# Kernel optimization log

Hardware: AMD Instinct MI355X
Metric: run time of the kernel (lower is better)

Reference implementation:

```python
import jax, jax.numpy as jnp
import numpy as np
import math

B, S, D, H, DFF = 4, 1024, 1024, 16, 4096
DK = D // H
EPS = 1e-6


def setup_inputs() -> dict:
    key = jax.random.key(0)
    ks = jax.random.split(key, 8)
    sc = 1.0 / math.sqrt(D)
    return {
        "x": jax.random.normal(ks[0], (B, S, D), jnp.float32),
        "src_mask": jnp.ones((B, 1, 1, S), jnp.int32),
        "wq": jax.random.normal(ks[1], (D, D), jnp.float32) * sc,
        "bq": jnp.zeros((D,), jnp.float32),
        "wk": jax.random.normal(ks[2], (D, D), jnp.float32) * sc,
        "bk": jnp.zeros((D,), jnp.float32),
        "wv": jax.random.normal(ks[3], (D, D), jnp.float32) * sc,
        "bv": jnp.zeros((D,), jnp.float32),
        "wo": jax.random.normal(ks[4], (D, D), jnp.float32) * sc,
        "bo": jnp.zeros((D,), jnp.float32),
        "w1": jax.random.normal(ks[5], (D, DFF), jnp.float32) * sc,
        "b1": jnp.zeros((DFF,), jnp.float32),
        "w2": jax.random.normal(ks[6], (DFF, D), jnp.float32) * (1.0 / math.sqrt(DFF)),
        "b2": jnp.zeros((D,), jnp.float32),
        "alpha1": jnp.ones((1,), jnp.float32),
        "beta1": jnp.zeros((1,), jnp.float32),
        "alpha2": jnp.ones((1,), jnp.float32),
        "beta2": jnp.zeros((1,), jnp.float32),
    }


def layer_norm(x, alpha, beta):
    # Faithful to the custom LayerNormalization: scalar alpha/beta,
    # torch std (unbiased, ddof=1), eps added to std (not variance).
    mean = jnp.mean(x, axis=-1, keepdims=True)
    std = jnp.std(x, axis=-1, keepdims=True, ddof=1)
    return alpha * (x - mean) / (std + EPS) + beta


def encoder_block(x, src_mask, wq, bq, wk, bk, wv, bv, wo, bo,
                  w1, b1, w2, b2, alpha1, beta1, alpha2, beta2):
    # --- residual 1: pre-norm self-attention (dropout = 0 / eval mode) ---
    xn = layer_norm(x, alpha1, beta1)
    q = (xn @ wq + bq).reshape(B, S, H, DK).transpose(0, 2, 1, 3)  # bhsd
    k = (xn @ wk + bk).reshape(B, S, H, DK).transpose(0, 2, 1, 3)
    v = (xn @ wv + bv).reshape(B, S, H, DK).transpose(0, 2, 1, 3)
    scores = jnp.einsum("bhqd,bhkd->bhqk", q, k) / math.sqrt(DK)
    scores = jnp.where(src_mask == 0, jnp.float32(-1e9), scores)
    attn = jax.nn.softmax(scores, axis=-1)
    ctx = jnp.einsum("bhqk,bhkd->bhqd", attn, v)
    ctx = ctx.transpose(0, 2, 1, 3).reshape(B, S, D)
    x = x + (ctx @ wo + bo)
    # --- residual 2: pre-norm feed-forward ---
    xn2 = layer_norm(x, alpha2, beta2)
    ff = jax.nn.relu(xn2 @ w1 + b1) @ w2 + b2
    return x + ff


def reference(x, src_mask, wq, bq, wk, bk, wv, bv, wo, bo,
              w1, b1, w2, b2, alpha1, beta1, alpha2, beta2):
    return encoder_block(x, src_mask, wq, bq, wk, bk, wv, bv, wo, bo,
                         w1, b1, w2, b2, alpha1, beta1, alpha2, beta2)
```

## Files before the change

### kernel.cpp

```cpp
#include <hip/hip_runtime.h>
#include <hip/hip_bf16.h>
#include <stdint.h>


typedef unsigned short u16;
typedef __attribute__((ext_vector_type(4))) float f32x4;
typedef __attribute__((ext_vector_type(8))) short bf16x8;
typedef __attribute__((ext_vector_type(4))) unsigned short u16x4;

__device__ __forceinline__ u16 f2b(float f) {
  unsigned int u = __builtin_bit_cast(unsigned int, f);
  u += 0x7FFFu + ((u >> 16) & 1u);
  return (u16)(u >> 16);
}

__device__ __forceinline__ void gload_lds16(const void* g, void* l) {
  __builtin_amdgcn_global_load_lds(
      reinterpret_cast<__attribute__((address_space(1))) void*>(
          reinterpret_cast<uintptr_t>(g)),
      reinterpret_cast<__attribute__((address_space(3))) void*>(
          reinterpret_cast<uintptr_t>(l)),
      16, 0, 0);
}

#define MFMA16(a, b, c) __builtin_amdgcn_mfma_f32_16x16x32_bf16((a), (b), (c), 0, 0, 0)

__global__ __launch_bounds__(256) void cast_transpose(
    const float* __restrict__ in, u16* __restrict__ out, int K, int N) {
  __shared__ float tile[32][33];
  const int n0 = blockIdx.x * 32, k0 = blockIdx.y * 32;
  const int tx = threadIdx.x & 31, ty = threadIdx.x >> 5;
#pragma unroll
  for (int i = 0; i < 32; i += 8)
    tile[ty + i][tx] = in[(int64_t)(k0 + ty + i) * N + (n0 + tx)];
  __syncthreads();
#pragma unroll
  for (int i = 0; i < 32; i += 8)
    out[(int64_t)(n0 + ty + i) * K + (k0 + tx)] = f2b(tile[tx][ty + i]);
}

__global__ void pack_bias(const float* __restrict__ bq, const float* __restrict__ bk,
                          const float* __restrict__ bv, float* __restrict__ out) {
  int i = blockIdx.x * 256 + threadIdx.x;
  const float* src = (i < 1024) ? bq : (i < 2048 ? bk : bv);
  out[i] = src[i & 1023];
}

__global__ __launch_bounds__(256) void transpose_v(
    const u16* __restrict__ qkv, u16* __restrict__ vt) {
  __shared__ u16 t[32][33];
  const int bh = blockIdx.z;
  const int b = bh >> 4, h = bh & 15;
  const int s0 = blockIdx.x * 32, d0 = blockIdx.y * 32;
  const int tx = threadIdx.x & 31, ty = threadIdx.x >> 5;
  const u16* src = qkv + (int64_t)(b * 1024) * 3072 + 2048 + h * 64;
#pragma unroll
  for (int i = 0; i < 32; i += 8)
    t[ty + i][tx] = src[(int64_t)(s0 + ty + i) * 3072 + d0 + tx];
  __syncthreads();
  u16* dst = vt + (int64_t)bh * 64 * 1024;
#pragma unroll
  for (int i = 0; i < 32; i += 8)
    dst[(int64_t)(d0 + ty + i) * 1024 + s0 + tx] = t[tx][ty + i];
}

__global__ __launch_bounds__(256) void layernorm_k(
    const float* __restrict__ x, const float* __restrict__ alpha,
    const float* __restrict__ beta, u16* __restrict__ out) {
  const int row = blockIdx.x;
  const float4 v = ((const float4*)(x + (int64_t)row * 1024))[threadIdx.x];
  float s = v.x + v.y + v.z + v.w;
  float sq = v.x * v.x + v.y * v.y + v.z * v.z + v.w * v.w;
#pragma unroll
  for (int off = 1; off < 64; off <<= 1) {
    s += __shfl_xor(s, off, 64);
    sq += __shfl_xor(sq, off, 64);
  }
  __shared__ float ss[4], ssq[4];
  const int wid = threadIdx.x >> 6;
  if ((threadIdx.x & 63) == 0) { ss[wid] = s; ssq[wid] = sq; }
  __syncthreads();
  s = ss[0] + ss[1] + ss[2] + ss[3];
  sq = ssq[0] + ssq[1] + ssq[2] + ssq[3];
  const float mean = s * (1.0f / 1024.0f);
  float var = (sq - 1024.0f * mean * mean) * (1.0f / 1023.0f);
  var = fmaxf(var, 0.0f);
  const float inv = alpha[0] / (sqrtf(var) + 1e-6f);
  const float bt = beta[0];
  u16x4 o;
  o[0] = f2b((v.x - mean) * inv + bt);
  o[1] = f2b((v.y - mean) * inv + bt);
  o[2] = f2b((v.z - mean) * inv + bt);
  o[3] = f2b((v.w - mean) * inv + bt);
  *(u16x4*)(out + (int64_t)row * 1024 + threadIdx.x * 4) = o;
}

template <int BN, bool OUT_BF16, bool RELU, bool RES>
__global__ __launch_bounds__(256) void gemm_bt(
    const u16* __restrict__ A, const u16* __restrict__ Bt,
    const float* __restrict__ bias, const float* __restrict__ res,
    void* __restrict__ Cout, int Ndim, int K) {
  constexpr int NF = BN / 32;
  __shared__ u16 Alds[128 * 32];
  __shared__ u16 Blds[BN * 32];
  const int tid = threadIdx.x;
  const int wid = tid >> 6, lane = tid & 63;
  const int bm0 = blockIdx.y * 128, bn0 = blockIdx.x * BN;
  const int wm = (wid >> 1) * 64, wn = (wid & 1) * (BN / 2);
  const int lrow = lane & 15, lg = lane >> 4;

  f32x4 acc[4][NF] = {};

  const int srow = tid >> 2;
  const int skoff = (tid & 3) * 8;
  const u16* Ag = A + (int64_t)(bm0 + srow) * K + skoff;
  const u16* Bg = Bt + (int64_t)(bn0 + srow) * K + skoff;
  char* AldsB0 = (char*)Alds + wid * 64 * 16;
  char* AldsB1 = (char*)Alds + (256 + wid * 64) * 16;
  char* BldsB0 = (char*)Blds + wid * 64 * 16;
  char* BldsB1 = (char*)Blds + (256 + wid * 64) * 16;
  const int64_t half = (int64_t)64 * K;

  const int nK = K >> 5;
  for (int kt = 0; kt < nK; ++kt) {
    __syncthreads();
    gload_lds16(Ag, AldsB0);
    gload_lds16(Ag + half, AldsB1);
    gload_lds16(Bg, BldsB0);
    if (BN == 128) gload_lds16(Bg + half, BldsB1);
    Ag += 32; Bg += 32;
    __syncthreads();
    bf16x8 af[4], bfr[NF];
#pragma unroll
    for (int f = 0; f < 4; ++f)
      af[f] = *(const bf16x8*)&Alds[(wm + f * 16 + lrow) * 32 + lg * 8];
#pragma unroll
    for (int f = 0; f < NF; ++f)
      bfr[f] = *(const bf16x8*)&Blds[(wn + f * 16 + lrow) * 32 + lg * 8];
#pragma unroll
    for (int mf = 0; mf < 4; ++mf)
#pragma unroll
      for (int nf = 0; nf < NF; ++nf)
        acc[mf][nf] = MFMA16(af[mf], bfr[nf], acc[mf][nf]);
  }

#pragma unroll
  for (int mf = 0; mf < 4; ++mf) {
#pragma unroll
    for (int nf = 0; nf < NF; ++nf) {
      const int col = bn0 + wn + nf * 16 + lrow;
      const float bv = bias[col];
#pragma unroll
      for (int r = 0; r < 4; ++r) {
        const int row = bm0 + wm + mf * 16 + lg * 4 + r;
        float v = acc[mf][nf][r] + bv;
        if (RELU) v = fmaxf(v, 0.0f);
        if (RES) v += res[(int64_t)row * Ndim + col];
        if (OUT_BF16)
          ((u16*)Cout)[(int64_t)row * Ndim + col] = f2b(v);
        else
          ((float*)Cout)[(int64_t)row * Ndim + col] = v;
      }
    }
  }
}

__global__ __launch_bounds__(256) void attention_k(
    const u16* __restrict__ qkv, const u16* __restrict__ vt,
    const int* __restrict__ mask, u16* __restrict__ ctxout) {
  const int bh = blockIdx.y;
  const int b = bh >> 4, h = bh & 15;
  const int q0 = blockIdx.x * 64;
  const int tid = threadIdx.x, wid = tid >> 6, lane = tid & 63;
  const int lrow = lane & 15, lg = lane >> 4;

  __shared__ u16 Klds[64 * 64];
  __shared__ u16 Vtlds[64 * 64];
  __shared__ u16 Plds[4][16 * 68];

  const int64_t rs = 3072;
  const u16* Qb = qkv + (int64_t)(b * 1024) * rs + h * 64;
  const u16* Kb = Qb + 1024;
  const u16* Vtb = vt + (int64_t)bh * 64 * 1024;

  bf16x8 qf[2];
  {
    const u16* qp = Qb + (int64_t)(q0 + wid * 16 + lrow) * rs + lg * 8;
    qf[0] = *(const bf16x8*)qp;
    qf[1] = *(const bf16x8*)(qp + 32);
  }

  const int c0 = wid * 64 + lane, c1 = 256 + c0;
  const int r0 = c0 >> 3, r1 = c1 >> 3;
  const int gq0 = (c0 & 7) ^ (r0 & 7), gq1 = (c1 & 7) ^ (r1 & 7);
  char* KldsB0 = (char*)Klds + wid * 64 * 16;
  char* KldsB1 = (char*)Klds + (256 + wid * 64) * 16;
  char* VldsB0 = (char*)Vtlds + wid * 64 * 16;
  char* VldsB1 = (char*)Vtlds + (256 + wid * 64) * 16;
  const u16* Kg0 = Kb + (int64_t)r0 * rs + gq0 * 8;
  const u16* Kg1 = Kb + (int64_t)r1 * rs + gq1 * 8;
  const u16* Vg0 = Vtb + r0 * 1024 + gq0 * 8;
  const u16* Vg1 = Vtb + r1 * 1024 + gq1 * 8;

  float m[4], l[4];
  f32x4 ctx[4] = {};
#pragma unroll
  for (int r = 0; r < 4; ++r) { m[r] = -1e30f; l[r] = 0.0f; }

  for (int kt = 0; kt < 16; ++kt) {
    const int sk0 = kt * 64;
    __syncthreads();
    gload_lds16(Kg0 + (int64_t)sk0 * rs, KldsB0);
    gload_lds16(Kg1 + (int64_t)sk0 * rs, KldsB1);
    gload_lds16(Vg0 + sk0, VldsB0);
    gload_lds16(Vg1 + sk0, VldsB1);
    __syncthreads();

    f32x4 sa[4];
#pragma unroll
    for (int nf = 0; nf < 4; ++nf) {
      const int srow = nf * 16 + lrow;
      const char* kr = (const char*)Klds + srow * 128;
      bf16x8 kf0 = *(const bf16x8*)(kr + ((lg ^ (srow & 7)) * 16));
      bf16x8 kf1 = *(const bf16x8*)(kr + (((4 | lg) ^ (srow & 7)) * 16));
      f32x4 a = {};
      a = MFMA16(qf[0], kf0, a);
      a = MFMA16(qf[1], kf1, a);
      sa[nf] = a;
    }
#pragma unroll
    for (int nf = 0; nf < 4; ++nf) {
      const int mval = mask[b * 1024 + sk0 + nf * 16 + lrow];
#pragma unroll
      for (int r = 0; r < 4; ++r) {
        const float sv = sa[nf][r] * 0.125f;
        sa[nf][r] = (mval == 0) ? -1e9f : sv;
      }
    }
    float fac[4];
#pragma unroll
    for (int r = 0; r < 4; ++r) {
      float mx = fmaxf(fmaxf(sa[0][r], sa[1][r]), fmaxf(sa[2][r], sa[3][r]));
#pragma unroll
      for (int off = 1; off < 16; off <<= 1) mx = fmaxf(mx, __shfl_xor(mx, off, 64));
      const float mn = fmaxf(m[r], mx);
      fac[r] = __expf(m[r] - mn);
      m[r] = mn;
    }
    float rsum[4] = {0.f, 0.f, 0.f, 0.f};
    u16 pb[4][4];
#pragma unroll
    for (int nf = 0; nf < 4; ++nf)
#pragma unroll
      for (int r = 0; r < 4; ++r) {
        const float p = __expf(sa[nf][r] - m[r]);
        rsum[r] += p;
        pb[nf][r] = f2b(p);
      }
#pragma unroll
    for (int r = 0; r < 4; ++r) {
      float t = rsum[r];
#pragma unroll
      for (int off = 1; off < 16; off <<= 1) t += __shfl_xor(t, off, 64);
      l[r] = l[r] * fac[r] + t;
#pragma unroll
      for (int df = 0; df < 4; ++df) ctx[df][r] *= fac[r];
    }
    u16* P = &Plds[wid][0];
#pragma unroll
    for (int nf = 0; nf < 4; ++nf)
#pragma unroll
      for (int r = 0; r < 4; ++r)
        P[(lg * 4 + r) * 68 + nf * 16 + lrow] = pb[nf][r];
    bf16x8 pf0 = *(const bf16x8*)&P[lrow * 68 + lg * 8];
    bf16x8 pf1 = *(const bf16x8*)&P[lrow * 68 + 32 + lg * 8];
#pragma unroll
    for (int df = 0; df < 4; ++df) {
      const int drow = df * 16 + lrow;
      const char* vr = (const char*)Vtlds + drow * 128;
      bf16x8 vf0 = *(const bf16x8*)(vr + ((lg ^ (drow & 7)) * 16));
      bf16x8 vf1 = *(const bf16x8*)(vr + (((4 | lg) ^ (drow & 7)) * 16));
      ctx[df] = MFMA16(pf0, vf0, ctx[df]);
      ctx[df] = MFMA16(pf1, vf1, ctx[df]);
    }
  }
#pragma unroll
  for (int df = 0; df < 4; ++df)
#pragma unroll
    for (int r = 0; r < 4; ++r) {
      const int row = b * 1024 + q0 + wid * 16 + lg * 4 + r;
      const int col = h * 64 + df * 16 + lrow;
      ctxout[(int64_t)row * 1024 + col] = f2b(ctx[df][r] / l[r]);
    }
}

extern "C" void kernel_launch(void* const* d_in, const int* in_sizes, int n_in,
                              void* d_out, int out_size, void* d_ws, size_t ws_size,
                              hipStream_t stream) {
  (void)in_sizes; (void)n_in; (void)out_size; (void)ws_size;
  const float* x      = (const float*)d_in[0];
  const int*   mask   = (const int*)d_in[1];
  const float* wq     = (const float*)d_in[2];
  const float* bq     = (const float*)d_in[3];
  const float* wk     = (const float*)d_in[4];
  const float* bk     = (const float*)d_in[5];
  const float* wv     = (const float*)d_in[6];
  const float* bv     = (const float*)d_in[7];
  const float* wo     = (const float*)d_in[8];
  const float* bo     = (const float*)d_in[9];
  const float* w1     = (const float*)d_in[10];
  const float* b1     = (const float*)d_in[11];
  const float* w2     = (const float*)d_in[12];
  const float* b2     = (const float*)d_in[13];
  const float* alpha1 = (const float*)d_in[14];
  const float* beta1  = (const float*)d_in[15];
  const float* alpha2 = (const float*)d_in[16];
  const float* beta2  = (const float*)d_in[17];
  float* out = (float*)d_out;

  char* ws = (char*)d_ws;
  u16*   wqkvT = (u16*)ws;                 ws += (size_t)3072 * 1024 * 2;
  u16*   woT   = (u16*)ws;                 ws += (size_t)1024 * 1024 * 2;
  u16*   w1T   = (u16*)ws;                 ws += (size_t)4096 * 1024 * 2;
  u16*   w2T   = (u16*)ws;                 ws += (size_t)1024 * 4096 * 2;
  float* bqkv  = (float*)ws;               ws += 16384;
  u16*   xn    = (u16*)ws;                 ws += (size_t)4096 * 1024 * 2;
  u16*   qkv   = (u16*)ws;                 ws += (size_t)4096 * 3072 * 2;
  u16*   ctx   = (u16*)ws;                 ws += (size_t)4096 * 1024 * 2;
  float* x2    = (float*)ws;               ws += (size_t)4096 * 1024 * 4;
  u16*   vtb   = (u16*)ws;                 ws += (size_t)64 * 64 * 1024 * 2;
  u16*   hbuf  = qkv;

  const dim3 blk(256);
  cast_transpose<<<dim3(32, 32), blk, 0, stream>>>(wq, wqkvT, 1024, 1024);
  cast_transpose<<<dim3(32, 32), blk, 0, stream>>>(wk, wqkvT + 1024 * 1024, 1024, 1024);
  cast_transpose<<<dim3(32, 32), blk, 0, stream>>>(wv, wqkvT + 2048 * 1024, 1024, 1024);
  cast_transpose<<<dim3(32, 32), blk, 0, stream>>>(wo, woT, 1024, 1024);
  cast_transpose<<<dim3(128, 32), blk, 0, stream>>>(w1, w1T, 1024, 4096);
  cast_transpose<<<dim3(32, 128), blk, 0, stream>>>(w2, w2T, 4096, 1024);
  pack_bias<<<dim3(12), blk, 0, stream>>>(bq, bk, bv, bqkv);
  layernorm_k<<<4096, blk, 0, stream>>>(x, alpha1, beta1, xn);
  gemm_bt<128, true, false, false><<<dim3(24, 32), blk, 0, stream>>>(
      xn, wqkvT, bqkv, nullptr, qkv, 3072, 1024);
  transpose_v<<<dim3(32, 2, 64), blk, 0, stream>>>(qkv, vtb);
  attention_k<<<dim3(16, 64), blk, 0, stream>>>(qkv, vtb, mask, ctx);
  gemm_bt<64, false, false, true><<<dim3(16, 32), blk, 0, stream>>>(
      ctx, woT, bo, x, x2, 1024, 1024);
  layernorm_k<<<4096, blk, 0, stream>>>(x2, alpha2, beta2, xn);
  gemm_bt<128, true, true, false><<<dim3(32, 32), blk, 0, stream>>>(
      xn, w1T, b1, nullptr, hbuf, 4096, 1024);
  gemm_bt<64, false, false, true><<<dim3(16, 32), blk, 0, stream>>>(
      hbuf, w2T, b2, x2, out, 1024, 4096);
}
```

Measured before the change: 415.5 us.

## Double-buffer GEMM LDS tiles and swizzle block order across XCDs

```diff
diff --git a/kernel.cpp b/kernel.cpp
--- a/kernel.cpp
+++ b/kernel.cpp
@@ -101,47 +101,55 @@
     const float* __restrict__ bias, const float* __restrict__ res,
     void* __restrict__ Cout, int Ndim, int K) {
   constexpr int NF = BN / 32;
-  __shared__ u16 Alds[128 * 32];
-  __shared__ u16 Blds[BN * 32];
+  __shared__ u16 Alds[2][128 * 32];
+  __shared__ u16 Blds[2][BN * 32];
   const int tid = threadIdx.x;
   const int wid = tid >> 6, lane = tid & 63;
-  const int bm0 = blockIdx.y * 128, bn0 = blockIdx.x * BN;
+  int flat = blockIdx.y * gridDim.x + blockIdx.x;
+  const int cpx = (gridDim.x * gridDim.y) >> 3;
+  flat = (flat & 7) * cpx + (flat >> 3);
+  const int bm0 = (flat / gridDim.x) * 128;
+  const int bn0 = (flat % gridDim.x) * BN;
   const int wm = (wid >> 1) * 64, wn = (wid & 1) * (BN / 2);
   const int lrow = lane & 15, lg = lane >> 4;
 
   f32x4 acc[4][NF] = {};
 
-  const int srow = tid >> 2;
-  const int skoff = (tid & 3) * 8;
+  const int srow = tid >> 2, skoff = (tid & 3) * 8;
   const u16* Ag = A + (int64_t)(bm0 + srow) * K + skoff;
   const u16* Bg = Bt + (int64_t)(bn0 + srow) * K + skoff;
-  char* AldsB0 = (char*)Alds + wid * 64 * 16;
-  char* AldsB1 = (char*)Alds + (256 + wid * 64) * 16;
-  char* BldsB0 = (char*)Blds + wid * 64 * 16;
-  char* BldsB1 = (char*)Blds + (256 + wid * 64) * 16;
   const int64_t half = (int64_t)64 * K;
 
+  auto stage = [&](int buf) {
+    char* ad = (char*)&Alds[buf][0] + tid * 16;
+    char* bd = (char*)&Blds[buf][0] + tid * 16;
+    gload_lds16(Ag, ad);
+    gload_lds16(Ag + half, ad + 4096);
+    gload_lds16(Bg, bd);
+    if (BN == 128) gload_lds16(Bg + half, bd + 4096);
+    Ag += 32; Bg += 32;
+  };
+
   const int nK = K >> 5;
+  stage(0);
+  __syncthreads();
+  int cur = 0;
   for (int kt = 0; kt < nK; ++kt) {
-    __syncthreads();
-    gload_lds16(Ag, AldsB0);
-    gload_lds16(Ag + half, AldsB1);
-    gload_lds16(Bg, BldsB0);
-    if (BN == 128) gload_lds16(Bg + half, BldsB1);
-    Ag += 32; Bg += 32;
-    __syncthreads();
+    if (kt + 1 < nK) stage(cur ^ 1);
     bf16x8 af[4], bfr[NF];
 #pragma unroll
     for (int f = 0; f < 4; ++f)
-      af[f] = *(const bf16x8*)&Alds[(wm + f * 16 + lrow) * 32 + lg * 8];
+      af[f] = *(const bf16x8*)&Alds[cur][(wm + f * 16 + lrow) * 32 + lg * 8];
 #pragma unroll
     for (int f = 0; f < NF; ++f)
-      bfr[f] = *(const bf16x8*)&Blds[(wn + f * 16 + lrow) * 32 + lg * 8];
+      bfr[f] = *(const bf16x8*)&Blds[cur][(wn + f * 16 + lrow) * 32 + lg * 8];
 #pragma unroll
     for (int mf = 0; mf < 4; ++mf)
 #pragma unroll
       for (int nf = 0; nf < NF; ++nf)
         acc[mf][nf] = MFMA16(af[mf], bfr[nf], acc[mf][nf]);
+    __syncthreads();
+    cur ^= 1;
   }
 
 #pragma unroll
```

Result: faster. 385.6 us (-7.2%).
